# Optimization experiments

Hardware: AMD Instinct MI355X
Metric: run time of the kernel (lower is better)

The kernel has to match this reference:

```python
import jax, jax.numpy as jnp
import numpy as np

EMBED_DIM = 1024
NUM_HEADS = 16
HEAD_DIM = EMBED_DIM // NUM_HEADS
L = 1024  # target/source seq len
N = 2     # batch
EPS = 1e-6


def setup_inputs() -> dict:
    key = jax.random.key(0)
    ks = jax.random.split(key, 11)
    s = 0.02
    return {
        "query": jax.random.normal(ks[0], (L, N, EMBED_DIM), jnp.float32),
        "key": jax.random.normal(ks[1], (L, N, EMBED_DIM), jnp.float32),
        "value": jax.random.normal(ks[2], (L, N, EMBED_DIM), jnp.float32),
        "Wq": jax.random.normal(ks[3], (EMBED_DIM, EMBED_DIM), jnp.float32) * s,
        "bq": jnp.zeros((EMBED_DIM,), jnp.float32),
        "Wk": jax.random.normal(ks[4], (EMBED_DIM, EMBED_DIM), jnp.float32) * s,
        "bk": jnp.zeros((EMBED_DIM,), jnp.float32),
        "Wv": jax.random.normal(ks[5], (EMBED_DIM, EMBED_DIM), jnp.float32) * s,
        "bv": jnp.zeros((EMBED_DIM,), jnp.float32),
        "Wo": jax.random.normal(ks[6], (EMBED_DIM, EMBED_DIM), jnp.float32) * s,
        "bo": jnp.zeros((EMBED_DIM,), jnp.float32),
    }


def _feature_map(x):
    # phi(x) = elu(x) + 1 (Katharopoulos et al., 2020)
    return jax.nn.elu(x) + 1.0


def reference(query, key, value, Wq, bq, Wk, bk, Wv, bv, Wo, bo):
    tgt_len, bsz, embed_dim = query.shape
    H, d = NUM_HEADS, HEAD_DIM
    # projections (torch Linear: x @ W.T + b)
    q = query @ Wq.T + bq
    k = key @ Wk.T + bk
    v = value @ Wv.T + bv
    # (L, N, E) -> (N*H, L, d)
    def to_heads(x):
        return x.reshape(-1, bsz * H, d).transpose(1, 0, 2)
    q, k, v = to_heads(q), to_heads(k), to_heads(v)
    q = _feature_map(q)
    k = _feature_map(k)
    # causal linear attention: S_t = cumsum_s<=t k_s v_s^T ; z_t = cumsum k_s
    kv = jnp.cumsum(jnp.einsum('bld,ble->blde', k, v), axis=1)  # (B*H, L, d, d)
    num = jnp.einsum('bld,blde->ble', q, kv)                    # (B*H, L, d)
    z = jnp.cumsum(k, axis=1)                                   # (B*H, L, d)
    denom = jnp.einsum('bld,bld->bl', q, z) + EPS               # (B*H, L)
    attn = num / denom[..., None]
    # (N*H, L, d) -> (L, N, E)
    attn = attn.transpose(1, 0, 2).reshape(tgt_len, bsz, embed_dim)
    return attn @ Wo.T + bo
```

## Files before the change

kernel.cpp:

```cpp
#include <hip/hip_runtime.h>
#include <cmath>


#define EPS 1e-6f

typedef short bf16x8 __attribute__((ext_vector_type(8)));
typedef float f32x4 __attribute__((ext_vector_type(4)));

__device__ __forceinline__ float b2f(ushort u) {
    union { unsigned u32; float f; } x; x.u32 = ((unsigned)u) << 16; return x.f;
}
__device__ __forceinline__ ushort f2b(float f) {
    union { float f; unsigned u; } x; x.f = f;
    unsigned r = (x.u + 0x7fffu + ((x.u >> 16) & 1u)) >> 16;
    return (ushort)r;
}
__device__ __forceinline__ void gload16(const void* g, void* l) {
    __builtin_amdgcn_global_load_lds(
        (__attribute__((address_space(1))) void*)(uintptr_t)g,
        (__attribute__((address_space(3))) void*)l,
        16, 0, 0);
}

template<int NSTEPS>
__device__ __forceinline__ void gemm_mainloop2(const ushort* __restrict__ A,
                                               const ushort* __restrict__ B,
                                               int brow, int bcol, int kbeg,
                                               ushort* Sh, f32x4 acc[4][4]) {
    const int K = 1024;
    const int BUF = 6144;
    int tid = threadIdx.x;
    int w = tid >> 6, lane = tid & 63;
    int fr = lane & 15, hi = lane >> 4;

    int srow = lane >> 2;
    int ssl  = lane & 3;
    int arowA = (w * 2) * 16 + srow;
    int arowB = (w * 4) * 16 + srow;
    const ushort* Ag = A + (size_t)(brow + arowA) * K + kbeg + ((ssl ^ ((arowA >> 1) & 3)) * 8);
    const ushort* Bg = B + (size_t)(bcol + arowB) * K + kbeg + ((ssl ^ ((arowB >> 1) & 3)) * 8);
    int adst = w * 1024;
    int bdst = 2048 + w * 2048;

    int fkey = (fr >> 1) & 3;
    int ea[4], eb[4];
    #pragma unroll
    for (int m = 0; m < 4; m++) ea[m] = (m * 16 + fr) * 32 + ((hi ^ fkey) * 8);
    #pragma unroll
    for (int n = 0; n < 4; n++) eb[n] = 2048 + (w * 64 + n * 16 + fr) * 32 + ((hi ^ fkey) * 8);

    #pragma unroll
    for (int m = 0; m < 4; m++)
        #pragma unroll
        for (int n = 0; n < 4; n++)
            acc[m][n] = (f32x4){0.f, 0.f, 0.f, 0.f};

    #pragma unroll
    for (int p = 0; p < 2; p++) {
        ushort* Sn = Sh + p * BUF;
        int k0 = p * 32;
        #pragma unroll
        for (int j = 0; j < 2; j++) gload16(Ag + k0 + (size_t)j * 16 * K, Sn + adst + j * 512);
        #pragma unroll
        for (int j = 0; j < 4; j++) gload16(Bg + k0 + (size_t)j * 16 * K, Sn + bdst + j * 512);
    }

    for (int t = 0; t < NSTEPS; ++t) {
        if (t + 2 < NSTEPS) {
            int k0 = (t + 2) * 32;
            ushort* Sn = Sh + ((t + 2) & 3) * BUF;
            #pragma unroll
            for (int j = 0; j < 2; j++) gload16(Ag + k0 + (size_t)j * 16 * K, Sn + adst + j * 512);
            #pragma unroll
            for (int j = 0; j < 4; j++) gload16(Bg + k0 + (size_t)j * 16 * K, Sn + bdst + j * 512);
        }
        if (t + 2 < NSTEPS)      asm volatile("s_waitcnt vmcnt(12)" ::: "memory");
        else if (t + 1 < NSTEPS) asm volatile("s_waitcnt vmcnt(6)" ::: "memory");
        else                     asm volatile("s_waitcnt vmcnt(0)" ::: "memory");
        __builtin_amdgcn_s_barrier();
        __builtin_amdgcn_sched_barrier(0);
        const ushort* Sc_ = Sh + (t & 3) * BUF;
        bf16x8 af[4], bf[4];
        #pragma unroll
        for (int m = 0; m < 4; m++) af[m] = *(const bf16x8*)&Sc_[ea[m]];
        #pragma unroll
        for (int n = 0; n < 4; n++) bf[n] = *(const bf16x8*)&Sc_[eb[n]];
        #pragma unroll
        for (int m = 0; m < 4; m++)
            #pragma unroll
            for (int n = 0; n < 4; n++)
                acc[m][n] = __builtin_amdgcn_mfma_f32_16x16x32_bf16(af[m], bf[n], acc[m][n], 0, 0, 0);
    }
}

__global__ __launch_bounds__(128) void gemm_proj(
    const ushort* __restrict__ Aq, const ushort* __restrict__ Ak, const ushort* __restrict__ Av,
    const ushort* __restrict__ Bq, const ushort* __restrict__ Bk, const ushort* __restrict__ Bv,
    const float* __restrict__ bq, const float* __restrict__ bk, const float* __restrict__ bv,
    ushort* __restrict__ oq, ushort* __restrict__ ok, ushort* __restrict__ ov) {
    __shared__ ushort Sh[4 * 6144];
    int z = blockIdx.z;
    const ushort* A = (z == 0) ? Aq : (z == 1) ? Ak : Av;
    const ushort* B = (z == 0) ? Bq : (z == 1) ? Bk : Bv;
    const float* bias = (z == 0) ? bq : (z == 1) ? bk : bv;
    int brow = blockIdx.y * 64, bcol = blockIdx.x * 128;
    f32x4 acc[4][4];
    gemm_mainloop2<32>(A, B, brow, bcol, 0, Sh, acc);
    int tid = threadIdx.x, w = tid >> 6, lane = tid & 63;
    int fr = lane & 15, hi = lane >> 4;
    #pragma unroll
    for (int m = 0; m < 4; m++)
        #pragma unroll
        for (int n = 0; n < 4; n++)
            #pragma unroll
            for (int r = 0; r < 4; r++) {
                int grow = brow + m * 16 + hi * 4 + r;
                int gcol = bcol + w * 64 + n * 16 + fr;
                float v = acc[m][n][r] + bias[gcol];
                int l = grow >> 1, nb2 = grow & 1, h = gcol >> 6, dd = gcol & 63;
                if (z == 2) {
                    ov[(size_t)((nb2 * 16 + h) * 64 + dd) * 1024 + l] = f2b(v);
                } else {
                    v = (v > 0.f) ? v + 1.f : __expf(v);
                    ushort* out = (z == 0) ? oq : ok;
                    out[(size_t)((nb2 * 16 + h) * 1024 + l) * 64 + dd] = f2b(v);
                }
            }
}

__global__ __launch_bounds__(128) void gemm_outk(const ushort* __restrict__ A,
                                                 const ushort* __restrict__ B,
                                                 float* __restrict__ pbuf) {
    __shared__ ushort Sh[4 * 6144];
    int brow = blockIdx.y * 64, bcol = blockIdx.x * 128, z = blockIdx.z;
    f32x4 acc[4][4];
    gemm_mainloop2<8>(A, B, brow, bcol, z * 256, Sh, acc);
    int tid = threadIdx.x, w = tid >> 6, lane = tid & 63;
    int fr = lane & 15, hi = lane >> 4;
    float* out = pbuf + (size_t)z * 2097152;
    #pragma unroll
    for (int m = 0; m < 4; m++)
        #pragma unroll
        for (int n = 0; n < 4; n++)
            #pragma unroll
            for (int r = 0; r < 4; r++) {
                int grow = brow + m * 16 + hi * 4 + r;
                int gcol = bcol + w * 64 + n * 16 + fr;
                out[(size_t)grow * 1024 + gcol] = acc[m][n][r];
            }
}

__global__ __launch_bounds__(256) void reduce_out(const float* __restrict__ p,
                                                  const float* __restrict__ bias,
                                                  float* __restrict__ out) {
    int i = blockIdx.x * 256 + threadIdx.x;
    float4 a = ((const float4*)p)[i];
    float4 b = ((const float4*)(p + 2097152))[i];
    float4 c = ((const float4*)(p + 4194304))[i];
    float4 d = ((const float4*)(p + 6291456))[i];
    float4 bb = ((const float4*)bias)[i & 255];
    float4 o;
    o.x = a.x + b.x + c.x + d.x + bb.x;
    o.y = a.y + b.y + c.y + d.y + bb.y;
    o.z = a.z + b.z + c.z + d.z + bb.z;
    o.w = a.w + b.w + c.w + d.w + bb.w;
    ((float4*)out)[i] = o;
}

__global__ __launch_bounds__(256) void cast_all(
    const float* __restrict__ i0, const float* __restrict__ i1, const float* __restrict__ i2,
    const float* __restrict__ i3, const float* __restrict__ i4, const float* __restrict__ i5,
    const float* __restrict__ i6,
    ushort* __restrict__ o0, ushort* __restrict__ o1, ushort* __restrict__ o2,
    ushort* __restrict__ o3, ushort* __restrict__ o4, ushort* __restrict__ o5,
    ushort* __restrict__ o6) {
    int z = blockIdx.z;
    const float* in = (z == 0) ? i0 : (z == 1) ? i1 : (z == 2) ? i2 :
                      (z == 3) ? i3 : (z == 4) ? i4 : (z == 5) ? i5 : i6;
    ushort* out = (z == 0) ? o0 : (z == 1) ? o1 : (z == 2) ? o2 :
                  (z == 3) ? o3 : (z == 4) ? o4 : (z == 5) ? o5 : o6;
    int n4 = (z < 3) ? 524288 : 262144;
    int i = blockIdx.x * 256 + threadIdx.x;
    if (i < n4) {
        float4 f = ((const float4*)in)[i];
        ushort4 o; o.x = f2b(f.x); o.y = f2b(f.y); o.z = f2b(f.z); o.w = f2b(f.w);
        ((ushort4*)out)[i] = o;
    }
}

__global__ __launch_bounds__(256) void chunk_sums(const ushort* __restrict__ kh,
                                                  const ushort* __restrict__ vt,
                                                  float* __restrict__ St,
                                                  float* __restrict__ zc) {
    int c = blockIdx.x, b = blockIdx.y, tid = threadIdx.x;
    __shared__ float Kl[64][64];
    __shared__ float Vl[64][65];
    const ushort* Kg = kh + (size_t)(b * 1024 + c * 64) * 64;
    for (int i = tid; i < 1024; i += 256) {
        ushort4 k4 = ((const ushort4*)Kg)[i];
        ((float4*)Kl)[i] = make_float4(b2f(k4.x), b2f(k4.y), b2f(k4.z), b2f(k4.w));
        int e = i >> 4, s4 = (i & 15) << 2;
        ushort4 v4 = *(const ushort4*)&vt[(size_t)(b * 64 + e) * 1024 + c * 64 + s4];
        Vl[e][s4 + 0] = b2f(v4.x); Vl[e][s4 + 1] = b2f(v4.y);
        Vl[e][s4 + 2] = b2f(v4.z); Vl[e][s4 + 3] = b2f(v4.w);
    }
    __syncthreads();
    int e = tid & 63, d0 = (tid >> 6) * 16;
    float s[16] = {};
    for (int ss = 0; ss < 64; ss++) {
        float ve = Vl[e][ss];
        #pragma unroll
        for (int i = 0; i < 16; i++) s[i] += Kl[ss][d0 + i] * ve;
    }
    float* So = St + (size_t)(b * 16 + c) * 4096 + e * 64 + d0;
    #pragma unroll
    for (int k = 0; k < 4; k++)
        *(float4*)&So[k * 4] = make_float4(s[4*k], s[4*k+1], s[4*k+2], s[4*k+3]);
    if (tid < 64) {
        float z = 0.f;
        for (int ss = 0; ss < 64; ss++) z += Kl[ss][tid];
        zc[(size_t)(b * 16 + c) * 64 + tid] = z;
    }
}

__global__ __launch_bounds__(256) void prefix_chunks(const float* __restrict__ St,
                                                     ushort* __restrict__ Spt,
                                                     float* __restrict__ zc) {
    int b = blockIdx.x, tid = threadIdx.x;
    size_t base = (size_t)b * 16 * 4096 + (size_t)tid * 16;
    float run[16] = {};
    for (int c = 0; c < 16; c++) {
        const float4* p4 = (const float4*)(St + base + (size_t)c * 4096);
        ushort* q = Spt + base + (size_t)c * 4096;
        #pragma unroll
        for (int k = 0; k < 4; k++) {
            float4 v = p4[k];
            ushort4 o;
            o.x = f2b(run[4*k+0]); o.y = f2b(run[4*k+1]);
            o.z = f2b(run[4*k+2]); o.w = f2b(run[4*k+3]);
            ((ushort4*)q)[k] = o;
            run[4*k+0] += v.x; run[4*k+1] += v.y; run[4*k+2] += v.z; run[4*k+3] += v.w;
        }
    }
    if (tid < 64) {
        float rz = 0.f;
        for (int c = 0; c < 16; c++) {
            size_t idx = ((size_t)b * 16 + c) * 64 + tid;
            float t = zc[idx];
            zc[idx] = rz;
            rz += t;
        }
    }
}

__global__ __launch_bounds__(256) void attn_chunk(const ushort* __restrict__ qh,
                                                  const ushort* __restrict__ kh,
                                                  const ushort* __restrict__ vt,
                                                  const ushort* __restrict__ Spt,
                                                  const float* __restrict__ zc,
                                                  ushort* __restrict__ attn) {
    int c = blockIdx.x, b = blockIdx.y, tid = threadIdx.x;
    int w = tid >> 6, lane = tid & 63;
    int fr = lane & 15, hi = lane >> 4;
    __shared__ ushort Q[4096], Kt[4096], VT[4096], SP[4096], P[4096];
    __shared__ float den[64];

    {
        const ushort* bases[4];
        bases[0] = qh + (size_t)(b * 1024 + c * 64) * 64;
        bases[1] = kh + (size_t)(b * 1024 + c * 64) * 64;
        bases[2] = vt;
        bases[3] = Spt + (size_t)(b * 16 + c) * 4096;
        ushort* dsts[4] = {Q, Kt, VT, SP};
        #pragma unroll
        for (int tl = 0; tl < 4; tl++) {
            #pragma unroll
            for (int j = 0; j < 2; j++) {
                int i = w * 64 + lane + 256 * j;
                int row = i >> 3, sl = i & 7;
                int col = (sl ^ (row & 7)) * 8;
                const ushort* src;
                if (tl == 2) src = vt + (size_t)(b * 64 + row) * 1024 + c * 64 + col;
                else         src = bases[tl] + (size_t)row * 64 + col;
                gload16(src, dsts[tl] + w * 512 + 2048 * j);
            }
        }
    }
    __syncthreads();

    int frow = w * 16 + fr;
    int fkey = fr & 7;
    bf16x8 aq[2];
    #pragma unroll
    for (int kk = 0; kk < 2; kk++)
        aq[kk] = *(const bf16x8*)&Q[frow * 64 + ((kk * 4 + hi) ^ fkey) * 8];
    f32x4 pc[4];
    #pragma unroll
    for (int n = 0; n < 4; n++) {
        pc[n] = (f32x4){0.f, 0.f, 0.f, 0.f};
        #pragma unroll
        for (int kk = 0; kk < 2; kk++) {
            bf16x8 bk_ = *(const bf16x8*)&Kt[(n * 16 + fr) * 64 + ((kk * 4 + hi) ^ fkey) * 8];
            pc[n] = __builtin_amdgcn_mfma_f32_16x16x32_bf16(aq[kk], bk_, pc[n], 0, 0, 0);
        }
    }
    float denp[4] = {0.f, 0.f, 0.f, 0.f};
    #pragma unroll
    for (int n = 0; n < 4; n++)
        #pragma unroll
        for (int r = 0; r < 4; r++) {
            int t = w * 16 + hi * 4 + r;
            int s = n * 16 + fr;
            float v = (s <= t) ? pc[n][r] : 0.f;
            denp[r] += v;
            P[t * 64 + (((s >> 3) ^ (t & 7)) * 8) + (s & 7)] = f2b(v);
        }
    #pragma unroll
    for (int r = 0; r < 4; r++) {
        denp[r] += __shfl_xor(denp[r], 1);
        denp[r] += __shfl_xor(denp[r], 2);
        denp[r] += __shfl_xor(denp[r], 4);
        denp[r] += __shfl_xor(denp[r], 8);
    }
    if (fr == 0) {
        #pragma unroll
        for (int r = 0; r < 4; r++) den[w * 16 + hi * 4 + r] = denp[r];
    }
    __syncthreads();

    if (tid < 64) {
        int t = tid;
        const float* zg = zc + (size_t)(b * 16 + c) * 64;
        float a = 0.f;
        for (int d = 0; d < 64; d++)
            a += b2f(Q[t * 64 + (((d >> 3) ^ (t & 7)) * 8) + (d & 7)]) * zg[d];
        den[t] += a;
    }

    bf16x8 ap[2];
    #pragma unroll
    for (int kk = 0; kk < 2; kk++)
        ap[kk] = *(const bf16x8*)&P[frow * 64 + ((kk * 4 + hi) ^ fkey) * 8];
    f32x4 nacc[4];
    #pragma unroll
    for (int n = 0; n < 4; n++) {
        nacc[n] = (f32x4){0.f, 0.f, 0.f, 0.f};
        #pragma unroll
        for (int kk = 0; kk < 2; kk++) {
            bf16x8 bs = *(const bf16x8*)&SP[(n * 16 + fr) * 64 + ((kk * 4 + hi) ^ fkey) * 8];
            nacc[n] = __builtin_amdgcn_mfma_f32_16x16x32_bf16(aq[kk], bs, nacc[n], 0, 0, 0);
        }
        #pragma unroll
        for (int kk = 0; kk < 2; kk++) {
            bf16x8 bv = *(const bf16x8*)&VT[(n * 16 + fr) * 64 + ((kk * 4 + hi) ^ fkey) * 8];
            nacc[n] = __builtin_amdgcn_mfma_f32_16x16x32_bf16(ap[kk], bv, nacc[n], 0, 0, 0);
        }
    }
    __syncthreads();

    int nb = b >> 4, h = b & 15;
    #pragma unroll
    for (int n = 0; n < 4; n++)
        #pragma unroll
        for (int r = 0; r < 4; r++) {
            int t = w * 16 + hi * 4 + r;
            int e = n * 16 + fr;
            int l = c * 64 + t;
            float val = nacc[n][r] / (den[t] + EPS);
            attn[(size_t)(l * 2 + nb) * 1024 + h * 64 + e] = f2b(val);
        }
}

extern "C" void kernel_launch(void* const* d_in, const int* in_sizes, int n_in,
                              void* d_out, int out_size, void* d_ws, size_t ws_size,
                              hipStream_t stream) {
    const float* query = (const float*)d_in[0];
    const float* key_  = (const float*)d_in[1];
    const float* value = (const float*)d_in[2];
    const float* Wq = (const float*)d_in[3];
    const float* bq = (const float*)d_in[4];
    const float* Wk = (const float*)d_in[5];
    const float* bk = (const float*)d_in[6];
    const float* Wv = (const float*)d_in[7];
    const float* bv = (const float*)d_in[8];
    const float* Wo = (const float*)d_in[9];
    const float* bo = (const float*)d_in[10];

    ushort* qbuf = (ushort*)d_ws;
    ushort* kbuf = qbuf + 2097152;
    ushort* vbuf = kbuf + 2097152;
    ushort* wqb  = vbuf + 2097152;
    ushort* wkb  = wqb + 1048576;
    ushort* wvb  = wkb + 1048576;
    ushort* wob  = wvb + 1048576;
    ushort* qh   = wob + 1048576;
    ushort* kh   = qh + 2097152;
    ushort* vt   = kh + 2097152;
    float*  St   = (float*)(vt + 2097152);
    ushort* Spt  = (ushort*)(St + 2097152);
    float*  zc   = (float*)(Spt + 2097152);
    float*  pbuf = zc + 32768;
    ushort* attn = qbuf;

    cast_all<<<dim3(2048, 1, 7), 256, 0, stream>>>(query, key_, value, Wq, Wk, Wv, Wo,
                                                   qbuf, kbuf, vbuf, wqb, wkb, wvb, wob);

    gemm_proj<<<dim3(8, 32, 3), 128, 0, stream>>>(qbuf, kbuf, vbuf, wqb, wkb, wvb,
                                                  bq, bk, bv, qh, kh, vt);

    chunk_sums<<<dim3(16, 32), 256, 0, stream>>>(kh, vt, St, zc);
    prefix_chunks<<<32, 256, 0, stream>>>(St, Spt, zc);
    attn_chunk<<<dim3(16, 32), 256, 0, stream>>>(qh, kh, vt, Spt, zc, attn);

    gemm_outk<<<dim3(8, 32, 4), 128, 0, stream>>>(attn, wob, pbuf);
    reduce_out<<<2048, 256, 0, stream>>>(pbuf, bo, (float*)d_out);
}
```

Measured before the change: 92.22 us.

## Load A fragments directly to registers and halve split-K in output GEMM

The GEMM mainloop now reads the A operand straight from global memory into registers, one step ahead, instead of staging it through LDS. Only B tiles go through the LDS ring, which shrinks shared memory per block. The output projection moves from 4-way to 2-way split-K, so the partial-sum buffer traffic and the reduction work are halved. The cost is more scattered global loads for A and fewer blocks in the output GEMM.

```diff
diff --git a/kernel.cpp b/kernel.cpp
--- a/kernel.cpp
+++ b/kernel.cpp
@@ -23,31 +23,36 @@
 }
 
 template<int NSTEPS>
-__device__ __forceinline__ void gemm_mainloop2(const ushort* __restrict__ A,
+__device__ __forceinline__ void gemm_mainloop3(const ushort* __restrict__ A,
                                                const ushort* __restrict__ B,
                                                int brow, int bcol, int kbeg,
                                                ushort* Sh, f32x4 acc[4][4]) {
     const int K = 1024;
-    const int BUF = 6144;
+    const int BUF = 4096;
     int tid = threadIdx.x;
     int w = tid >> 6, lane = tid & 63;
     int fr = lane & 15, hi = lane >> 4;
 
-    int srow = lane >> 2;
-    int ssl  = lane & 3;
-    int arowA = (w * 2) * 16 + srow;
-    int arowB = (w * 4) * 16 + srow;
-    const ushort* Ag = A + (size_t)(brow + arowA) * K + kbeg + ((ssl ^ ((arowA >> 1) & 3)) * 8);
-    const ushort* Bg = B + (size_t)(bcol + arowB) * K + kbeg + ((ssl ^ ((arowB >> 1) & 3)) * 8);
-    int adst = w * 1024;
-    int bdst = 2048 + w * 2048;
+    const ushort* Bg[4];
+    int bdst[4];
+    #pragma unroll
+    for (int j = 0; j < 4; j++) {
+        int slot = (j * 2 + w) * 64 + lane;
+        int row = slot >> 2, c16 = slot & 3;
+        Bg[j] = B + (size_t)(bcol + row) * K + kbeg + ((c16 ^ ((row >> 1) & 3)) * 8);
+        bdst[j] = (j * 2 + w) * 512;
+    }
+
+    const ushort* Ag[4];
+    #pragma unroll
+    for (int m = 0; m < 4; m++)
+        Ag[m] = A + (size_t)(brow + m * 16 + fr) * K + kbeg + hi * 8;
 
     int fkey = (fr >> 1) & 3;
-    int ea[4], eb[4];
-    #pragma unroll
-    for (int m = 0; m < 4; m++) ea[m] = (m * 16 + fr) * 32 + ((hi ^ fkey) * 8);
-    #pragma unroll
-    for (int n = 0; n < 4; n++) eb[n] = 2048 + (w * 64 + n * 16 + fr) * 32 + ((hi ^ fkey) * 8);
+    int eb[4];
+    #pragma unroll
+    for (int n = 0; n < 4; n++)
+        eb[n] = (w * 64 + n * 16 + fr) * 32 + ((hi ^ fkey) * 8);
 
     #pragma unroll
     for (int m = 0; m < 4; m++)
@@ -55,41 +60,42 @@
         for (int n = 0; n < 4; n++)
             acc[m][n] = (f32x4){0.f, 0.f, 0.f, 0.f};
 
-    #pragma unroll
-    for (int p = 0; p < 2; p++) {
-        ushort* Sn = Sh + p * BUF;
-        int k0 = p * 32;
-        #pragma unroll
-        for (int j = 0; j < 2; j++) gload16(Ag + k0 + (size_t)j * 16 * K, Sn + adst + j * 512);
-        #pragma unroll
-        for (int j = 0; j < 4; j++) gload16(Bg + k0 + (size_t)j * 16 * K, Sn + bdst + j * 512);
-    }
+    bf16x8 afc[4], afn[4];
+    #pragma unroll
+    for (int m = 0; m < 4; m++) afc[m] = *(const bf16x8*)(Ag[m]);
+    #pragma unroll
+    for (int p = 0; p < 2; p++)
+        #pragma unroll
+        for (int j = 0; j < 4; j++)
+            gload16(Bg[j] + p * 32, Sh + p * BUF + bdst[j]);
 
     for (int t = 0; t < NSTEPS; ++t) {
+        if (t + 1 < NSTEPS) {
+            #pragma unroll
+            for (int m = 0; m < 4; m++) afn[m] = *(const bf16x8*)(Ag[m] + (t + 1) * 32);
+        }
         if (t + 2 < NSTEPS) {
             int k0 = (t + 2) * 32;
             ushort* Sn = Sh + ((t + 2) & 3) * BUF;
             #pragma unroll
-            for (int j = 0; j < 2; j++) gload16(Ag + k0 + (size_t)j * 16 * K, Sn + adst + j * 512);
-            #pragma unroll
-            for (int j = 0; j < 4; j++) gload16(Bg + k0 + (size_t)j * 16 * K, Sn + bdst + j * 512);
+            for (int j = 0; j < 4; j++) gload16(Bg[j] + k0, Sn + bdst[j]);
         }
         if (t + 2 < NSTEPS)      asm volatile("s_waitcnt vmcnt(12)" ::: "memory");
-        else if (t + 1 < NSTEPS) asm volatile("s_waitcnt vmcnt(6)" ::: "memory");
+        else if (t + 1 < NSTEPS) asm volatile("s_waitcnt vmcnt(8)" ::: "memory");
         else                     asm volatile("s_waitcnt vmcnt(0)" ::: "memory");
         __builtin_amdgcn_s_barrier();
         __builtin_amdgcn_sched_barrier(0);
-        const ushort* Sc_ = Sh + (t & 3) * BUF;
-        bf16x8 af[4], bf[4];
-        #pragma unroll
-        for (int m = 0; m < 4; m++) af[m] = *(const bf16x8*)&Sc_[ea[m]];
-        #pragma unroll
-        for (int n = 0; n < 4; n++) bf[n] = *(const bf16x8*)&Sc_[eb[n]];
+        const ushort* Bc = Sh + (t & 3) * BUF;
+        bf16x8 bf[4];
+        #pragma unroll
+        for (int n = 0; n < 4; n++) bf[n] = *(const bf16x8*)&Bc[eb[n]];
         #pragma unroll
         for (int m = 0; m < 4; m++)
             #pragma unroll
             for (int n = 0; n < 4; n++)
-                acc[m][n] = __builtin_amdgcn_mfma_f32_16x16x32_bf16(af[m], bf[n], acc[m][n], 0, 0, 0);
+                acc[m][n] = __builtin_amdgcn_mfma_f32_16x16x32_bf16(afc[m], bf[n], acc[m][n], 0, 0, 0);
+        #pragma unroll
+        for (int m = 0; m < 4; m++) afc[m] = afn[m];
     }
 }
 
@@ -98,14 +104,14 @@
     const ushort* __restrict__ Bq, const ushort* __restrict__ Bk, const ushort* __restrict__ Bv,
     const float* __restrict__ bq, const float* __restrict__ bk, const float* __restrict__ bv,
     ushort* __restrict__ oq, ushort* __restrict__ ok, ushort* __restrict__ ov) {
-    __shared__ ushort Sh[4 * 6144];
+    __shared__ ushort Sh[4 * 4096];
     int z = blockIdx.z;
     const ushort* A = (z == 0) ? Aq : (z == 1) ? Ak : Av;
     const ushort* B = (z == 0) ? Bq : (z == 1) ? Bk : Bv;
     const float* bias = (z == 0) ? bq : (z == 1) ? bk : bv;
     int brow = blockIdx.y * 64, bcol = blockIdx.x * 128;
     f32x4 acc[4][4];
-    gemm_mainloop2<32>(A, B, brow, bcol, 0, Sh, acc);
+    gemm_mainloop3<32>(A, B, brow, bcol, 0, Sh, acc);
     int tid = threadIdx.x, w = tid >> 6, lane = tid & 63;
     int fr = lane & 15, hi = lane >> 4;
     #pragma unroll
@@ -131,10 +137,10 @@
 __global__ __launch_bounds__(128) void gemm_outk(const ushort* __restrict__ A,
                                                  const ushort* __restrict__ B,
                                                  float* __restrict__ pbuf) {
-    __shared__ ushort Sh[4 * 6144];
+    __shared__ ushort Sh[4 * 4096];
     int brow = blockIdx.y * 64, bcol = blockIdx.x * 128, z = blockIdx.z;
     f32x4 acc[4][4];
-    gemm_mainloop2<8>(A, B, brow, bcol, z * 256, Sh, acc);
+    gemm_mainloop3<16>(A, B, brow, bcol, z * 512, Sh, acc);
     int tid = threadIdx.x, w = tid >> 6, lane = tid & 63;
     int fr = lane & 15, hi = lane >> 4;
     float* out = pbuf + (size_t)z * 2097152;
@@ -156,14 +162,12 @@
     int i = blockIdx.x * 256 + threadIdx.x;
     float4 a = ((const float4*)p)[i];
     float4 b = ((const float4*)(p + 2097152))[i];
-    float4 c = ((const float4*)(p + 4194304))[i];
-    float4 d = ((const float4*)(p + 6291456))[i];
     float4 bb = ((const float4*)bias)[i & 255];
     float4 o;
-    o.x = a.x + b.x + c.x + d.x + bb.x;
-    o.y = a.y + b.y + c.y + d.y + bb.y;
-    o.z = a.z + b.z + c.z + d.z + bb.z;
-    o.w = a.w + b.w + c.w + d.w + bb.w;
+    o.x = a.x + b.x + bb.x;
+    o.y = a.y + b.y + bb.y;
+    o.z = a.z + b.z + bb.z;
+    o.w = a.w + b.w + bb.w;
     ((float4*)out)[i] = o;
 }
 
@@ -412,6 +416,6 @@
     prefix_chunks<<<32, 256, 0, stream>>>(St, Spt, zc);
     attn_chunk<<<dim3(16, 32), 256, 0, stream>>>(qh, kh, vt, Spt, zc, attn);
 
-    gemm_outk<<<dim3(8, 32, 4), 128, 0, stream>>>(attn, wob, pbuf);
+    gemm_outk<<<dim3(8, 32, 2), 128, 0, stream>>>(attn, wob, pbuf);
     reduce_out<<<2048, 256, 0, stream>>>(pbuf, bo, (float*)d_out);
 }
```

After: 101.7 us. 10.2% more time.
